# Kernel optimization log

Hardware: AMD Instinct MI355X
Metric: run time of the kernel (lower is better)

The kernel has to match this reference:

```python
import jax, jax.numpy as jnp
import numpy as np

B, V, N = 256, 50, 32
D, H, L, CS, NN, OUT = 128, 384, 12, 10, 10000, 128
ND = N * D          # per-visit input dim
G = 4 * H + 2 * L   # gate projection width
CH = H // L         # chunk size
HS = H // 6         # scale bottleneck


def setup_inputs() -> dict:
    key = jax.random.key(0)
    ks = jax.random.split(key, 20)
    s = 0.02
    embed = jax.random.normal(ks[0], (NN + 1, D), jnp.float32) * s
    embed = embed.at[0].set(0.0)  # padding_idx=0
    inp = {
        'node_ids': jax.random.randint(ks[1], (B, V, N), 0, NN + 1),
        'edge_idx': jax.random.randint(ks[2], (2, 128), 0, NN),
        'edge_attr': jax.random.normal(ks[3], (128,), jnp.float32),
        'time': jax.random.uniform(ks[4], (B, V), jnp.float32),
        'visit_order': jax.random.randint(ks[5], (B, V), 0, V),
        'attn_mask': jnp.ones((B, V), jnp.bool_),
        'embed': embed,
        'kernel_w': jax.random.normal(ks[6], (G, ND + 1), jnp.float32) * s,
        'kernel_b': jnp.zeros((G,), jnp.float32),
        'rec_w': jax.random.normal(ks[7], (G, H + 1), jnp.float32) * s,
        'rec_b': jnp.zeros((G,), jnp.float32),
        'scale_w': jax.random.normal(ks[8], (HS, H), jnp.float32) * s,
        'scale_b': jnp.zeros((HS,), jnp.float32),
        'rescale_w': jax.random.normal(ks[9], (H, HS), jnp.float32) * s,
        'rescale_b': jnp.zeros((H,), jnp.float32),
        'conv_w': jax.random.normal(ks[10], (H, H, CS), jnp.float32) * s,
        'conv_b': jnp.zeros((H,), jnp.float32),
        'out_w': jax.random.normal(ks[11], (OUT, V * H), jnp.float32) * s,
        'out_b': jnp.zeros((OUT,), jnp.float32),
    }
    return inp


def _cumax_l2r(x):
    return jnp.cumsum(jax.nn.softmax(x, -1), -1)


def _cumax_r2l(x):
    return jnp.flip(jnp.cumsum(jax.nn.softmax(jnp.flip(x, -1), -1), -1), -1)


def _forward(node_ids, time, embed, kernel_w, kernel_b, rec_w, rec_b,
             scale_w, scale_b, rescale_w, rescale_b, conv_w, conv_b, out_w, out_b):
    x = embed[node_ids].reshape(B, V, ND)  # gather per-visit code embeddings

    def step(carry, xs):
        c, h, tmp_h, tmp_dis = carry
        x_t, t_t = xs
        iv = t_t[:, None]
        xo = (jnp.concatenate([x_t, iv], -1) @ kernel_w.T + kernel_b
              + jnp.concatenate([h, iv], -1) @ rec_w.T + rec_b)
        fm = _cumax_l2r(xo[:, :L])              # [B,L] master forget
        im = _cumax_r2l(xo[:, L:2 * L])         # [B,L] master input
        g = xo[:, 2 * L:].reshape(B, 4 * L, CH)
        f = jax.nn.sigmoid(g[:, :L])
        i_ = jax.nn.sigmoid(g[:, L:2 * L])
        o = jax.nn.sigmoid(g[:, 2 * L:3 * L])
        cin = jnp.tanh(g[:, 3 * L:])
        cl = c.reshape(B, L, CH)
        fmE, imE = fm[:, :, None], im[:, :, None]
        ov = fmE * imE
        cnew = ov * (f * cl + i_ * cin) + (fmE - ov) * cl + (imE - ov) * cin
        hnew = (o * jnp.tanh(cnew)).reshape(B, H)
        cnew = cnew.reshape(B, H)
        dist = 1.0 - jnp.mean(fm, -1)           # [B]
        tmp_h = jnp.concatenate([tmp_h[1:], hnew[None]], 0)    # [CS,B,H]
        tmp_dis = jnp.concatenate([tmp_dis[1:], dist[None]], 0)  # [CS,B]
        ld = jax.nn.softmax(jnp.cumsum(tmp_dis.T, 1), 1)       # [B,CS]
        lh = tmp_h.transpose(1, 2, 0) * ld[:, None, :]         # [B,H,CS]
        theme = jax.nn.sigmoid(
            jnp.maximum(jnp.mean(lh, -1) @ scale_w.T + scale_b, 0.0)
            @ rescale_w.T + rescale_b)
        conv = jnp.einsum('bhk,ohk->bo', lh, conv_w) + conv_b  # valid conv, len 1
        local = theme * conv
        return (cnew, hnew, tmp_h, tmp_dis), (local, hnew, dist)

    c0 = jnp.zeros((B, H), jnp.float32)
    h0 = jnp.zeros((B, H), jnp.float32)
    tmp_h0 = jnp.zeros((CS, B, H), jnp.float32)
    tmp_dis0 = jnp.zeros((CS, B), jnp.float32)
    xs = (x.transpose(1, 0, 2), time.T)
    _, (hs, ohs, dists) = jax.lax.scan(step, (c0, h0, tmp_h0, tmp_dis0), xs)
    rnn = hs.transpose(1, 0, 2) + ohs.transpose(1, 0, 2)       # [B,V,H]
    out = rnn.reshape(B, V * H) @ out_w.T + out_b
    return out, dists  # dists: [V,B]


def reference(node_ids, edge_idx, edge_attr, time, visit_order, attn_mask,
              embed, kernel_w, kernel_b, rec_w, rec_b, scale_w, scale_b,
              rescale_w, rescale_b, conv_w, conv_b, out_w, out_b):
    # edge_idx / edge_attr / visit_order / attn_mask are unused by StageNet.forward
    return _forward(node_ids, time, embed, kernel_w, kernel_b, rec_w, rec_b,
                    scale_w, scale_b, rescale_w, rescale_b, conv_w, conv_b,
                    out_w, out_b)
```

## Files before the change

### kernel.cpp

```cpp
#include <hip/hip_runtime.h>
#include <math.h>

typedef _Float16 f16;
typedef _Float16 f16x8 __attribute__((ext_vector_type(8)));
typedef float f32x4 __attribute__((ext_vector_type(4)));
typedef unsigned int u32;
typedef u32 u32x4 __attribute__((ext_vector_type(4)));

#define DEV static __device__ __forceinline__

DEV float sigm(float x)  { return 1.0f / (1.0f + __expf(-x)); }
DEV float tanhfast(float x) { return 2.0f / (1.0f + __expf(-2.0f * x)) - 1.0f; }

DEV void gld16(const void* g, void* l) {
  __builtin_amdgcn_global_load_lds((const __attribute__((address_space(1))) void*)g,
                                   (__attribute__((address_space(3))) void*)l, 16, 0, 0);
}

DEV void gbar(int* bar, int nblk) {
  __syncthreads();
  if (threadIdx.x == 0) {
    int* cnt = bar;
    int* gen = bar + 16;
    int g = __hip_atomic_load(gen, __ATOMIC_RELAXED, __HIP_MEMORY_SCOPE_AGENT);
    int a = __hip_atomic_fetch_add(cnt, 1, __ATOMIC_RELEASE, __HIP_MEMORY_SCOPE_AGENT);
    if (a == nblk - 1) {
      __hip_atomic_store(cnt, 0, __ATOMIC_RELAXED, __HIP_MEMORY_SCOPE_AGENT);
      __hip_atomic_store(gen, g + 1, __ATOMIC_RELEASE, __HIP_MEMORY_SCOPE_AGENT);
    } else {
      while (__hip_atomic_load(gen, __ATOMIC_RELAXED, __HIP_MEMORY_SCOPE_AGENT) == g)
        __builtin_amdgcn_s_sleep(1);
    }
    (void)__hip_atomic_load(gen, __ATOMIC_ACQUIRE, __HIP_MEMORY_SCOPE_AGENT);
  }
  __syncthreads();
}

#define GP 1664
#define KH 3840
#define KO 19200
#define NGRP 16
#define NMEM 12
#define NBLK 192
#define XOLS 164
#define RECUR_LDS (122880 + 10496 + 1024)

static constexpr size_t OFF_OPART = 0;
static constexpr size_t OFF_ZB    = 104857600 - 262144;
static constexpr size_t OFF_WK    = 104857600;
static constexpr size_t OFF_XK    = OFF_WK + 13631488;
static constexpr size_t OFF_MLH   = OFF_XK;
static constexpr size_t OFF_S1    = OFF_XK + 9830400;
static constexpr size_t OFF_TH    = OFF_XK + 13107200;
static constexpr size_t OFF_CV    = OFF_XK + 32768000;
static constexpr size_t OFF_SWP   = OFF_XK + 72089600;
static constexpr size_t OFF_RWP2  = OFF_XK + 72187904;
static constexpr size_t OFF_SBP   = OFF_XK + 72286208;
static constexpr size_t OFF_RW    = OFF_XK + 85196800;
static constexpr size_t OFF_SV    = OFF_RW + 1474560;
static constexpr size_t OFF_BAR   = OFF_SV + 8192;
static constexpr size_t OFF_BIASC = OFF_BAR + 32768;
static constexpr size_t OFF_HALL  = OFF_BIASC + 8192;
static constexpr size_t OFF_LD    = OFF_HALL + 9830400;
static constexpr size_t OFF_WC2   = OFF_LD + 512000;
static constexpr size_t OFF_RNN   = OFF_WC2 + 2949120;
static constexpr size_t OFF_OUTW  = OFF_RNN + 9830400;
static constexpr size_t OFF_EH    = OFF_OUTW + 4915200;


__global__ __launch_bounds__(256) void k_prep_wk(const float* __restrict__ kw,
                                                 const float* __restrict__ kb,
                                                 const float* __restrict__ rb,
                                                 f16* __restrict__ Wk,
                                                 float* __restrict__ biasc) {
  long i = (long)blockIdx.x * 256 + threadIdx.x;
  if (i < 1664L * 4096) {
    int nn = (int)(i >> 12);
    int k  = (int)(i & 4095);
    float v = (nn < 1560) ? kw[(long)nn * 4097 + k] : 0.0f;
    Wk[i] = (f16)v;
  }
  if (i < 1664) biasc[i] = (i < 1560) ? (kb[i] + rb[i]) : 0.0f;
}

__global__ __launch_bounds__(512) void k_prep_misc(const float* __restrict__ rw,
                                                   const float* __restrict__ kw,
                                                   const float* __restrict__ sw,
                                                   const float* __restrict__ sb,
                                                   const float* __restrict__ rw2,
                                                   const float* __restrict__ cw,
                                                   const float* __restrict__ ow,
                                                   const float* __restrict__ embed,
                                                   f16* __restrict__ RWp,
                                                   float* __restrict__ Sv,
                                                   int* __restrict__ bar,
                                                   f16* __restrict__ swp,
                                                   float* __restrict__ sbp,
                                                   f16* __restrict__ rwp2,
                                                   f16* __restrict__ Wc2,
                                                   f16* __restrict__ outw,
                                                   f16* __restrict__ Eh) {
  const int blk = blockIdx.x, tid = threadIdx.x;
  if (blk < 180) {
    int i = blk * 512 + tid;
    if (i < 92160) {
      int p = i / 7680;
      int rem = i - p * 7680;
      int tau = rem / 768;
      int r2 = rem - tau * 768;
      int f = r2 >> 6;
      int l = r2 & 63;
      int lc = tau * 16 + (l & 15);
      int n;
      if (lc < 24) n = lc;
      else if (lc < 32) n = -1;
      else { int run = (lc - 32) >> 5; n = 24 + (run * 12 + p) * 32 + ((lc - 32) & 31); }
      int k = f * 32 + ((l >> 4) << 3);
      f16x8 o;
      if (n >= 0) {
        const float* s = rw + (long)n * 385 + k;
#pragma unroll
        for (int e = 0; e < 8; ++e) o[e] = (f16)s[e];
      } else {
#pragma unroll
        for (int e = 0; e < 8; ++e) o[e] = (f16)0.0f;
      }
      *(f16x8*)(RWp + (long)i * 8) = o;
    }
    if (i < 1664)
      Sv[i] = (i < 1560) ? (rw[(long)i * 385 + 384] + kw[(long)i * 4097 + 4096]) : 0.0f;
    if (i < 8192) bar[i] = 0;
  } else if (blk < 276) {
    int i = (blk - 180) * 512 + tid;
    if (i < 128 * 384) {
      int o = i / 384, k = i - o * 384;
      swp[i] = (f16)((o < 64) ? sw[o * 384 + k] : 0.0f);
      int o2 = i >> 7, k2 = i & 127;
      rwp2[i] = (f16)((k2 < 64) ? rw2[o2 * 64 + k2] : 0.0f);
    }
    if (i < 128) sbp[i] = (i < 64) ? sb[i] : 0.0f;
  } else if (blk < 3156) {
    int i = (blk - 276) * 512 + tid;
    if (i < 384 * 3840) {
      int o = i / 3840;
      int c = i - o * 3840;
      int j = c / 384;
      int h = c - j * 384;
      Wc2[i] = (f16)cw[((long)o * 384 + h) * 10 + j];
    }
  } else if (blk < 7956) {
    long i = (long)(blk - 3156) * 512 + tid;
    if (i < 128L * KO) outw[i] = (f16)ow[i];
  } else {
    long i = (long)(blk - 7956) * 512 + tid;
    if (i < 10001L * 128) Eh[i] = (f16)embed[i];
  }
}

__global__ __launch_bounds__(256) void k_gemm_emb(const int* __restrict__ ids,
                                                  const f16* __restrict__ Eh,
                                                  const f16* __restrict__ W,
                                                  f16* __restrict__ C,
                                                  const float* __restrict__ bias) {
  __shared__ __align__(16) f16 As[128 * 32];
  __shared__ __align__(16) f16 Bs[128 * 32];
  const int tid = threadIdx.x;
  const int W0  = blockIdx.y * 100 + blockIdx.x;
  const int xcd = W0 & 7, idx = W0 >> 3;
  const int nw  = (xcd < 4) ? (xcd * 163 + idx) : (652 + (xcd - 4) * 162 + idx);
  const int bx  = nw % 100, by = nw / 100;
  const long rowA0 = (long)bx * 128;
  const long rowB0 = (long)by * 128;
  const int w = tid >> 6, lane = tid & 63;
  const int q = lane >> 4, r16 = lane & 15;
  const int wr = w >> 1, wc = w & 1;
  f32x4 acc[4][4] = {};
  const int srow = tid >> 2;
  const int scol = (tid & 3) * 8;
  const int* idr0 = ids + (rowA0 + srow) * 32;
  const int* idr1 = ids + (rowA0 + srow + 64) * 32;
  const f16* gB0 = W + (rowB0 + srow) * 4096L + scol;
  const f16* gB1 = gB0 + 64L * 4096;
  f16* lA = As + tid * 8;
  f16* lB = Bs + tid * 8;
  int cur0 = idr0[0], cur1 = idr1[0];
  for (int n = 0; n < 32; ++n) {
    int nx0 = 0, nx1 = 0;
    if (n < 31) { nx0 = idr0[n + 1]; nx1 = idr1[n + 1]; }
#pragma unroll
    for (int kk = 0; kk < 4; ++kk) {
      const int k0 = n * 128 + kk * 32;
      const int d = kk * 32 + scol;
      __syncthreads();
      gld16(Eh + (size_t)cur0 * 128 + d, lA);
      gld16(Eh + (size_t)cur1 * 128 + d, lA + 2048);
      gld16(gB0 + k0, lB);
      gld16(gB1 + k0, lB + 2048);
      __syncthreads();
      f16x8 af[4], bfr[4];
#pragma unroll
      for (int i = 0; i < 4; i++) {
        af[i]  = *(const f16x8*)&As[(wr * 64 + i * 16 + r16) * 32 + q * 8];
        bfr[i] = *(const f16x8*)&Bs[(wc * 64 + i * 16 + r16) * 32 + q * 8];
      }
#pragma unroll
      for (int i = 0; i < 4; i++)
#pragma unroll
        for (int j = 0; j < 4; j++)
          acc[i][j] = __builtin_amdgcn_mfma_f32_16x16x32_f16(af[i], bfr[j], acc[i][j], 0, 0, 0);
    }
    cur0 = nx0; cur1 = nx1;
  }
#pragma unroll
  for (int i = 0; i < 4; i++)
#pragma unroll
    for (int j = 0; j < 4; j++) {
      long row = rowA0 + wr * 64 + i * 16 + q * 4;
      long col = rowB0 + wc * 64 + j * 16 + r16;
      float bv = bias[col];
#pragma unroll
      for (int r = 0; r < 4; r++)
        C[(row + r) * (long)GP + col] = (f16)(acc[i][j][r] + bv);
    }
}

__global__ __launch_bounds__(256) void k_gemm_conv(const float* __restrict__ ld,
                                                   const f16* __restrict__ h_all,
                                                   const f16* __restrict__ W,
                                                   float* __restrict__ C) {
  __shared__ __align__(16) f16 As[128 * 32];
  __shared__ __align__(16) f16 Bs[128 * 32];
  const int tid = threadIdx.x;
  const long rowA0 = (long)blockIdx.x * 128;
  const long rowB0 = (long)blockIdx.y * 128;
  const int ks = blockIdx.z * 1920;
  const long zoff = (long)blockIdx.z * (12800L * 384);
  const int w = tid >> 6, lane = tid & 63;
  const int q = lane >> 4, r16 = lane & 15;
  const int wr = w >> 1, wc = w & 1;
  f32x4 acc[4][4] = {};
  const int srow = tid >> 2;
  const int scol = (tid & 3) * 8;
  const int row0 = (int)rowA0 + srow, row1 = row0 + 64;
  const int b0r = row0 / 50, t0r = row0 - b0r * 50;
  const int b1r = row1 / 50, t1r = row1 - b1r * 50;
  const f16* gB0 = W + (rowB0 + srow) * (long)KH + ks + scol;
  const f16* gB1 = gB0 + 64L * KH;
  f16* lB = Bs + tid * 8;
  for (int k0 = 0; k0 < 1920; k0 += 32) {
    const int col0 = ks + k0;
    const int j = col0 / 384;
    const int hh = col0 - j * 384 + scol;
    const int s0 = t0r - 9 + j, s1 = t1r - 9 + j;
    __syncthreads();
    gld16(gB0 + k0, lB);
    gld16(gB1 + k0, lB + 2048);
    f16x8 a0v = {}, a1v = {};
    if (s0 >= 0) {
      const float lv = ld[row0 * 10 + j];
      f16x8 hv = *(const f16x8*)(h_all + ((size_t)s0 * 256 + b0r) * 384 + hh);
#pragma unroll
      for (int e = 0; e < 8; ++e) a0v[e] = (f16)((float)hv[e] * lv);
    }
    if (s1 >= 0) {
      const float lv = ld[row1 * 10 + j];
      f16x8 hv = *(const f16x8*)(h_all + ((size_t)s1 * 256 + b1r) * 384 + hh);
#pragma unroll
      for (int e = 0; e < 8; ++e) a1v[e] = (f16)((float)hv[e] * lv);
    }
    *(f16x8*)&As[srow * 32 + scol] = a0v;
    *(f16x8*)&As[(srow + 64) * 32 + scol] = a1v;
    __syncthreads();
    f16x8 af[4], bfr[4];
#pragma unroll
    for (int i = 0; i < 4; i++) {
      af[i]  = *(const f16x8*)&As[(wr * 64 + i * 16 + r16) * 32 + q * 8];
      bfr[i] = *(const f16x8*)&Bs[(wc * 64 + i * 16 + r16) * 32 + q * 8];
    }
#pragma unroll
    for (int i = 0; i < 4; i++)
#pragma unroll
      for (int j2 = 0; j2 < 4; j2++)
        acc[i][j2] = __builtin_amdgcn_mfma_f32_16x16x32_f16(af[i], bfr[j2], acc[i][j2], 0, 0, 0);
  }
#pragma unroll
  for (int i = 0; i < 4; i++)
#pragma unroll
    for (int j2 = 0; j2 < 4; j2++) {
      long row = rowA0 + wr * 64 + i * 16 + q * 4;
      long col = rowB0 + wc * 64 + j2 * 16 + r16;
#pragma unroll
      for (int r = 0; r < 4; r++)
        C[(row + r) * 384L + col + zoff] = acc[i][j2][r];
    }
}

__global__ __launch_bounds__(256) void k_gemm_bt(const f16* __restrict__ A,
                                                 const f16* __restrict__ W,
                                                 void* __restrict__ Cv,
                                                 const float* __restrict__ bias,
                                                 int N, int K, int kLen, int act) {
  __shared__ __align__(16) f16 As[128 * 32];
  __shared__ __align__(16) f16 Bs[128 * 32];
  const int tid = threadIdx.x;
  const long rowA0 = (long)blockIdx.x * 128;
  const long rowB0 = (long)blockIdx.y * 128;
  const long ks = (long)blockIdx.z * kLen;
  const long zoff = (long)blockIdx.z * ((long)gridDim.x * 128 * N);
  const int w = tid >> 6, lane = tid & 63;
  const int q = lane >> 4, r16 = lane & 15;
  const int wr = w >> 1, wc = w & 1;
  f32x4 acc[4][4] = {};
  const int srow = tid >> 2;
  const int scol = (tid & 3) * 8;
  const f16* gA0 = A + (rowA0 + srow) * (long)K + ks + scol;
  const f16* gA1 = gA0 + 64L * K;
  const f16* gB0 = W + (rowB0 + srow) * (long)K + ks + scol;
  const f16* gB1 = gB0 + 64L * K;
  f16* lA = As + tid * 8;
  f16* lB = Bs + tid * 8;
  for (int k0 = 0; k0 < kLen; k0 += 32) {
    __syncthreads();
    gld16(gA0 + k0, lA);
    gld16(gA1 + k0, lA + 2048);
    gld16(gB0 + k0, lB);
    gld16(gB1 + k0, lB + 2048);
    __syncthreads();
    f16x8 af[4], bfr[4];
#pragma unroll
    for (int i = 0; i < 4; i++) {
      af[i]  = *(const f16x8*)&As[(wr * 64 + i * 16 + r16) * 32 + q * 8];
      bfr[i] = *(const f16x8*)&Bs[(wc * 64 + i * 16 + r16) * 32 + q * 8];
    }
#pragma unroll
    for (int i = 0; i < 4; i++)
#pragma unroll
      for (int j = 0; j < 4; j++)
        acc[i][j] = __builtin_amdgcn_mfma_f32_16x16x32_f16(af[i], bfr[j], acc[i][j], 0, 0, 0);
  }
#pragma unroll
  for (int i = 0; i < 4; i++)
#pragma unroll
    for (int j = 0; j < 4; j++) {
      long row = rowA0 + wr * 64 + i * 16 + q * 4;
      long col = rowB0 + wc * 64 + j * 16 + r16;
      float bv = bias ? bias[col] : 0.0f;
#pragma unroll
      for (int r = 0; r < 4; r++) {
        float v = acc[i][j][r] + bv;
        long off = (row + r) * (long)N + col + zoff;
        if (act == 0)      ((float*)Cv)[off] = v;
        else if (act == 1) ((f16*)Cv)[off]   = (f16)v;
        else if (act == 2) ((f16*)Cv)[off]   = (f16)fmaxf(v, 0.0f);
        else               ((float*)Cv)[off] = sigm(v);
      }
    }
}

__global__ __launch_bounds__(640)
void k_recur_coop(const f16* __restrict__ XKh,
                  const f16* __restrict__ RWp,
                  const float* __restrict__ Sv,
                  const float* __restrict__ timep,
                  f16* __restrict__ zbuf,
                  f16* __restrict__ hall,
                  float* __restrict__ dists,
                  int* __restrict__ bar) {
  extern __shared__ char smem[];
  f16*   Wl  = (f16*)smem;
  float* xol = (float*)(smem + 122880);
  f16*   hl  = (f16*)(smem + 122880 + 10496);
  const int tid = threadIdx.x;
  const int g = blockIdx.x / NMEM;
  const int m = blockIdx.x - g * NMEM;
  const int b0 = g * 16;
  int* gflags = bar + g * 256;
  int* ibar   = bar + 4096 + g * 32;
  const int w = tid >> 6, lane = tid & 63;
  const int q = lane >> 4, r16 = lane & 15;
  {
    const f16* src = RWp + (size_t)m * 61440;
    for (int i = tid; i < 7680; i += 640)
      *(f16x8*)(Wl + (size_t)i * 8) = *(const f16x8*)(src + (size_t)i * 8);
  }
  int ncol = -1; float Svc = 0.0f;
  if (w < 10) {
    const int lc = w * 16 + r16;
    if (lc < 24) ncol = lc;
    else if (lc >= 32) { int run = (lc - 32) >> 5; ncol = 24 + (run * 12 + m) * 32 + ((lc - 32) & 31); }
    if (ncol >= 0) Svc = Sv[ncol];
  }
  {
    f16x8 z = {};
    for (int i = m * 640 + tid; i < 768; i += NMEM * 640)
      *(f16x8*)(zbuf + (size_t)b0 * 384 + (size_t)i * 8) = z;
  }
  gbar(ibar, NMEM);

  const int ch = tid & 31, bloc = tid >> 5;
  float creg = 0.0f;
  f16 xkc[4] = {};
  if (w < 10 && ncol >= 0) {
#pragma unroll
    for (int r = 0; r < 4; ++r)
      xkc[r] = XKh[((long)(b0 + q * 4 + r) * 50) * GP + ncol];
  }

  for (int t = 0; t < 50; ++t) {
    const f16* hprev = (t == 0) ? zbuf : (hall + (size_t)(t - 1) * 98304);
    f16 xkn[4] = {};
    if (w < 10) {
      f16x8 af[12];
      const f16* ab = hprev + (size_t)(b0 + r16) * 384 + q * 8;
#pragma unroll
      for (int f = 0; f < 12; ++f) af[f] = *(const f16x8*)(ab + f * 32);
      if (t < 49 && ncol >= 0) {
#pragma unroll
        for (int r = 0; r < 4; ++r)
          xkn[r] = XKh[((long)(b0 + q * 4 + r) * 50 + (t + 1)) * GP + ncol];
      }
      float tv4[4];
#pragma unroll
      for (int r = 0; r < 4; ++r) tv4[r] = timep[(b0 + q * 4 + r) * 50 + t];
      const f16* bp = Wl + (size_t)w * 6144 + lane * 8;
      f32x4 a0 = {};
#pragma unroll
      for (int f = 0; f < 12; ++f)
        a0 = __builtin_amdgcn_mfma_f32_16x16x32_f16(af[f], *(const f16x8*)(bp + f * 512), a0, 0, 0, 0);
      const int lc = w * 16 + r16;
#pragma unroll
      for (int r = 0; r < 4; ++r)
        xol[(q * 4 + r) * XOLS + lc] = a0[r] + (float)xkc[r] + tv4[r] * Svc;
    }
    __syncthreads();
    if (bloc < 16) {
      const int gb = b0 + bloc;
      const float* xr = xol + bloc * XOLS;
      float e1[12], e2[12], mx1 = -1e30f, mx2 = -1e30f;
#pragma unroll
      for (int l = 0; l < 12; ++l) {
        e1[l] = xr[l];      mx1 = fmaxf(mx1, e1[l]);
        e2[l] = xr[12 + l]; mx2 = fmaxf(mx2, e2[l]);
      }
      float s1 = 0.0f, s2 = 0.0f;
#pragma unroll
      for (int l = 0; l < 12; ++l) {
        e1[l] = __expf(e1[l] - mx1); s1 += e1[l];
        e2[l] = __expf(e2[l] - mx2); s2 += e2[l];
      }
      float cum1 = 0.0f;
      for (int l = 0; l <= m; ++l) cum1 += e1[l];
      const float fmv = cum1 / s1;
      float cum2 = 0.0f;
      for (int l = 11; l >= m; --l) cum2 += e2[l];
      const float imv = cum2 / s2;
      if (m == 0 && ch == 0) {
        float ds = 0.0f;
#pragma unroll
        for (int l = 0; l < 12; ++l) ds += (float)(12 - l) * e1[l];
        dists[t * 256 + gb] = 1.0f - ds / (12.0f * s1);
      }
      const float fv = sigm(xr[32 + ch]);
      const float iv = sigm(xr[64 + ch]);
      const float og = sigm(xr[96 + ch]);
      const float ci = tanhfast(xr[128 + ch]);
      const float ov = fmv * imv;
      const float cn = ov * (fv * creg + iv * ci) + (fmv - ov) * creg + (imv - ov) * ci;
      creg = cn;
      const float hv = og * tanhfast(cn);
      hl[tid] = (f16)hv;
    }
    __syncthreads();
    if (w == 0) {
      f32x4 d = *(const f32x4*)(hl + lane * 8);
      f16* dst = hall + ((size_t)t * 256 + b0 + (lane >> 2)) * 384 + m * 32 + (lane & 3) * 8;
      asm volatile("global_store_dwordx4 %0, %1, off sc0 sc1\n\t"
                   "s_waitcnt vmcnt(0)"
                   :: "v"(dst), "v"(d) : "memory");
      if (lane == 0) {
        int* fp = gflags + m * 16;
        int fv2 = t + 1;
        asm volatile("global_store_dword %0, %1, off sc0 sc1"
                     :: "v"(fp), "v"(fv2) : "memory");
      }
    }
    if (w == 1 && lane < NMEM) {
      while (__hip_atomic_load(gflags + lane * 16, __ATOMIC_RELAXED, __HIP_MEMORY_SCOPE_AGENT) < t + 1)
        __builtin_amdgcn_s_sleep(1);
    }
    __syncthreads();
    asm volatile("" ::: "memory");
#pragma unroll
    for (int r = 0; r < 4; ++r) xkc[r] = xkn[r];
  }
}

__global__ __launch_bounds__(256) void k_ld(const float* __restrict__ dists,
                                            float* __restrict__ ld) {
  int i = blockIdx.x * 256 + threadIdx.x;
  if (i >= 12800) return;
  int b = i / 50, t = i - b * 50;
  float v[10];
  float cum = 0.0f, mx = -1e30f;
#pragma unroll
  for (int j = 0; j < 10; j++) {
    int s = t - 9 + j;
    float d = (s >= 0) ? dists[s * 256 + b] : 0.0f;
    cum += d; v[j] = cum; mx = fmaxf(mx, cum);
  }
  float sum = 0.0f;
#pragma unroll
  for (int j = 0; j < 10; j++) { v[j] = __expf(v[j] - mx); sum += v[j]; }
  float inv = 1.0f / sum;
#pragma unroll
  for (int j = 0; j < 10; j++) ld[i * 10 + j] = v[j] * inv;
}

__global__ __launch_bounds__(256) void k_mlh(const float* __restrict__ ld,
                                             const f16* __restrict__ h_all,
                                             f16* __restrict__ mlh) {
  int i = blockIdx.x * 256 + threadIdx.x;
  int row = i / 384, h = i - row * 384;
  int b = row / 50, t = row - b * 50;
  float acc = 0.0f;
#pragma unroll
  for (int j = 0; j < 10; j++) {
    int s = t - 9 + j;
    if (s >= 0) acc += ld[row * 10 + j] * (float)h_all[((size_t)s * 256 + b) * 384 + h];
  }
  mlh[i] = (f16)(acc * 0.1f);
}

__global__ __launch_bounds__(256) void k_rnn(const float* __restrict__ theme,
                                             const float* __restrict__ convp,
                                             const float* __restrict__ cb,
                                             const f16* __restrict__ h_all,
                                             f16* __restrict__ rnn) {
  int i = blockIdx.x * 256 + threadIdx.x;
  int row = i / 384, h = i - row * 384;
  int b = row / 50, t = row - b * 50;
  float conv = convp[i] + convp[4915200 + i] + cb[h];
  float local = theme[i] * conv;
  float hv = (float)h_all[((size_t)t * 256 + b) * 384 + h];
  rnn[i] = (f16)(local + hv);
}

__global__ __launch_bounds__(256) void k_red8(const float* __restrict__ part,
                                              const float* __restrict__ ob,
                                              float* __restrict__ out) {
  int i = blockIdx.x * 256 + threadIdx.x;
  float s = 0.0f;
#pragma unroll
  for (int z = 0; z < 8; z++) s += part[z * 32768 + i];
  out[i] = s + ob[i & 127];
}

extern "C" void kernel_launch(void* const* d_in, const int* in_sizes, int n_in,
                              void* d_out, int out_size, void* d_ws, size_t ws_size,
                              hipStream_t stream) {
  (void)in_sizes; (void)n_in; (void)out_size; (void)ws_size;
  const int*   node_ids  = (const int*)  d_in[0];
  const float* timep     = (const float*)d_in[3];
  const float* embed     = (const float*)d_in[6];
  const float* kernel_w  = (const float*)d_in[7];
  const float* kernel_b  = (const float*)d_in[8];
  const float* rec_w     = (const float*)d_in[9];
  const float* rec_b     = (const float*)d_in[10];
  const float* scale_w   = (const float*)d_in[11];
  const float* scale_b   = (const float*)d_in[12];
  const float* rescale_w = (const float*)d_in[13];
  const float* rescale_b = (const float*)d_in[14];
  const float* conv_w    = (const float*)d_in[15];
  const float* conv_b    = (const float*)d_in[16];
  const float* out_w     = (const float*)d_in[17];
  const float* out_b     = (const float*)d_in[18];

  char* ws = (char*)d_ws;
  float* opart   = (float*)(ws + OFF_OPART);
  f16*   zbuf    = (f16*)  (ws + OFF_ZB);
  f16*   Wk      = (f16*)  (ws + OFF_WK);
  f16*   XKh     = (f16*)  (ws + OFF_XK);
  f16*   mlh_h   = (f16*)  (ws + OFF_MLH);
  f16*   s1h     = (f16*)  (ws + OFF_S1);
  float* theme   = (float*)(ws + OFF_TH);
  float* convbuf = (float*)(ws + OFF_CV);
  f16*   swp     = (f16*)  (ws + OFF_SWP);
  f16*   rwp2    = (f16*)  (ws + OFF_RWP2);
  float* sbp     = (float*)(ws + OFF_SBP);
  f16*   RWp     = (f16*)  (ws + OFF_RW);
  float* Sv      = (float*)(ws + OFF_SV);
  int*   bar     = (int*)  (ws + OFF_BAR);
  float* biasc   = (float*)(ws + OFF_BIASC);
  f16*   h_all   = (f16*)  (ws + OFF_HALL);
  float* ldbuf   = (float*)(ws + OFF_LD);
  f16*   Wc2     = (f16*)  (ws + OFF_WC2);
  f16*   rnn     = (f16*)  (ws + OFF_RNN);
  f16*   outw    = (f16*)  (ws + OFF_OUTW);
  f16*   Eh      = (f16*)  (ws + OFF_EH);

  float* outp  = (float*)d_out;
  float* dists = outp + 256 * 128;

  k_prep_wk  <<<26624, 256, 0, stream>>>(kernel_w, kernel_b, rec_b, Wk, biasc);
  k_prep_misc<<<10457, 512, 0, stream>>>(rec_w, kernel_w, scale_w, scale_b, rescale_w,
                                         conv_w, out_w, embed,
                                         RWp, Sv, bar, swp, sbp, rwp2, Wc2, outw, Eh);
  k_gemm_emb<<<dim3(100, 13), 256, 0, stream>>>(node_ids, Eh, Wk, XKh, biasc);
  {
    hipFuncSetAttribute((const void*)k_recur_coop,
                        hipFuncAttributeMaxDynamicSharedMemorySize, RECUR_LDS);
    void* cargs[] = {(void*)&XKh, (void*)&RWp, (void*)&Sv, (void*)&timep,
                     (void*)&zbuf, (void*)&h_all, (void*)&dists, (void*)&bar};
    hipLaunchCooperativeKernel((void*)k_recur_coop, dim3(NBLK), dim3(640),
                               cargs, RECUR_LDS, stream);
  }
  k_ld  <<<50,    256, 0, stream>>>(dists, ldbuf);
  k_mlh <<<19200, 256, 0, stream>>>(ldbuf, h_all, mlh_h);
  k_gemm_bt<<<dim3(100, 1), 256, 0, stream>>>(mlh_h, swp, s1h, sbp, 128, 384, 384, 2);
  k_gemm_bt<<<dim3(100, 3), 256, 0, stream>>>(s1h, rwp2, theme, rescale_b, 384, 128, 128, 3);
  k_gemm_conv<<<dim3(100, 3, 2), 256, 0, stream>>>(ldbuf, h_all, Wc2, convbuf);
  k_rnn <<<19200, 256, 0, stream>>>(theme, convbuf, conv_b, h_all, rnn);
  k_gemm_bt<<<dim3(2, 1, 8), 256, 0, stream>>>(rnn, outw, opart, nullptr, 128, KO, KO / 8, 0);
  k_red8<<<128, 256, 0, stream>>>(opart, out_b, outp);
}
```

Measured before the change: 977.2 us.

## Widen embedding GEMM K-step to 64 and raise output GEMM split-K to 40

The embedding-gather GEMM now loads two 32-wide K slabs per barrier pair into separate LDS buffers, halving the number of sync rounds per visit block. The final output projection GEMM moves from 8-way to 40-way split-K, so 80 blocks run instead of 16, and the reduction kernel sums 40 partials. This trades more LDS use and more partial-sum traffic for fewer barriers and more parallelism on a skinny GEMM.

```diff
diff --git a/kernel.cpp b/kernel.cpp
--- a/kernel.cpp
+++ b/kernel.cpp
@@ -39,6 +39,7 @@
 #define GP 1664
 #define KH 3840
 #define KO 19200
+#define ZSPLIT 40
 #define NGRP 16
 #define NMEM 12
 #define NBLK 192
@@ -162,8 +163,10 @@
                                                   const f16* __restrict__ W,
                                                   f16* __restrict__ C,
                                                   const float* __restrict__ bias) {
-  __shared__ __align__(16) f16 As[128 * 32];
-  __shared__ __align__(16) f16 Bs[128 * 32];
+  __shared__ __align__(16) f16 As0[128 * 32];
+  __shared__ __align__(16) f16 As1[128 * 32];
+  __shared__ __align__(16) f16 Bs0[128 * 32];
+  __shared__ __align__(16) f16 Bs1[128 * 32];
   const int tid = threadIdx.x;
   const int W0  = blockIdx.y * 100 + blockIdx.x;
   const int xcd = W0 & 7, idx = W0 >> 3;
@@ -181,27 +184,43 @@
   const int* idr1 = ids + (rowA0 + srow + 64) * 32;
   const f16* gB0 = W + (rowB0 + srow) * 4096L + scol;
   const f16* gB1 = gB0 + 64L * 4096;
-  f16* lA = As + tid * 8;
-  f16* lB = Bs + tid * 8;
+  f16* lA0 = As0 + tid * 8;
+  f16* lA1 = As1 + tid * 8;
+  f16* lB0 = Bs0 + tid * 8;
+  f16* lB1 = Bs1 + tid * 8;
   int cur0 = idr0[0], cur1 = idr1[0];
   for (int n = 0; n < 32; ++n) {
     int nx0 = 0, nx1 = 0;
     if (n < 31) { nx0 = idr0[n + 1]; nx1 = idr1[n + 1]; }
 #pragma unroll
-    for (int kk = 0; kk < 4; ++kk) {
-      const int k0 = n * 128 + kk * 32;
-      const int d = kk * 32 + scol;
+    for (int kk = 0; kk < 2; ++kk) {
+      const int k0 = n * 128 + kk * 64;
+      const int d = kk * 64 + scol;
       __syncthreads();
-      gld16(Eh + (size_t)cur0 * 128 + d, lA);
-      gld16(Eh + (size_t)cur1 * 128 + d, lA + 2048);
-      gld16(gB0 + k0, lB);
-      gld16(gB1 + k0, lB + 2048);
+      gld16(Eh + (size_t)cur0 * 128 + d,      lA0);
+      gld16(Eh + (size_t)cur1 * 128 + d,      lA0 + 2048);
+      gld16(Eh + (size_t)cur0 * 128 + d + 32, lA1);
+      gld16(Eh + (size_t)cur1 * 128 + d + 32, lA1 + 2048);
+      gld16(gB0 + k0,      lB0);
+      gld16(gB1 + k0,      lB0 + 2048);
+      gld16(gB0 + k0 + 32, lB1);
+      gld16(gB1 + k0 + 32, lB1 + 2048);
       __syncthreads();
       f16x8 af[4], bfr[4];
 #pragma unroll
       for (int i = 0; i < 4; i++) {
-        af[i]  = *(const f16x8*)&As[(wr * 64 + i * 16 + r16) * 32 + q * 8];
-        bfr[i] = *(const f16x8*)&Bs[(wc * 64 + i * 16 + r16) * 32 + q * 8];
+        af[i]  = *(const f16x8*)&As0[(wr * 64 + i * 16 + r16) * 32 + q * 8];
+        bfr[i] = *(const f16x8*)&Bs0[(wc * 64 + i * 16 + r16) * 32 + q * 8];
+      }
+#pragma unroll
+      for (int i = 0; i < 4; i++)
+#pragma unroll
+        for (int j = 0; j < 4; j++)
+          acc[i][j] = __builtin_amdgcn_mfma_f32_16x16x32_f16(af[i], bfr[j], acc[i][j], 0, 0, 0);
+#pragma unroll
+      for (int i = 0; i < 4; i++) {
+        af[i]  = *(const f16x8*)&As1[(wr * 64 + i * 16 + r16) * 32 + q * 8];
+        bfr[i] = *(const f16x8*)&Bs1[(wc * 64 + i * 16 + r16) * 32 + q * 8];
       }
 #pragma unroll
       for (int i = 0; i < 4; i++)
@@ -545,13 +564,13 @@
   rnn[i] = (f16)(local + hv);
 }
 
-__global__ __launch_bounds__(256) void k_red8(const float* __restrict__ part,
-                                              const float* __restrict__ ob,
-                                              float* __restrict__ out) {
+__global__ __launch_bounds__(256) void k_red(const float* __restrict__ part,
+                                             const float* __restrict__ ob,
+                                             float* __restrict__ out) {
   int i = blockIdx.x * 256 + threadIdx.x;
   float s = 0.0f;
 #pragma unroll
-  for (int z = 0; z < 8; z++) s += part[z * 32768 + i];
+  for (int z = 0; z < ZSPLIT; z++) s += part[z * 32768 + i];
   out[i] = s + ob[i & 127];
 }
 
@@ -620,6 +639,6 @@
   k_gemm_bt<<<dim3(100, 3), 256, 0, stream>>>(s1h, rwp2, theme, rescale_b, 384, 128, 128, 3);
   k_gemm_conv<<<dim3(100, 3, 2), 256, 0, stream>>>(ldbuf, h_all, Wc2, convbuf);
   k_rnn <<<19200, 256, 0, stream>>>(theme, convbuf, conv_b, h_all, rnn);
-  k_gemm_bt<<<dim3(2, 1, 8), 256, 0, stream>>>(rnn, outw, opart, nullptr, 128, KO, KO / 8, 0);
-  k_red8<<<128, 256, 0, stream>>>(opart, out_b, outp);
-}
+  k_gemm_bt<<<dim3(2, 1, ZSPLIT), 256, 0, stream>>>(rnn, outw, opart, nullptr, 128, KO, KO / ZSPLIT, 0);
+  k_red<<<128, 256, 0, stream>>>(opart, out_b, outp);
+}
```

Measured after the change: 936.8 us. 1.04x faster.
